# Performance work log

Hardware: AMD Instinct MI355X
Metric: run time of the kernel (lower is better)

Reference implementation:

```python
import jax, jax.numpy as jnp
import numpy as np

MARGIN = 0.3
K_AN = 3
K_AP = 6
KMAX = max(K_AN, K_AP)
NORMALIZE = True


def setup_inputs() -> dict:
    key = jax.random.key(0)
    k1, k2 = jax.random.split(key)
    inputs = jax.random.normal(k1, (128, 32, 128), dtype=jnp.float32)
    targets = jax.random.randint(k2, (128,), 0, 16, dtype=jnp.int64)
    return {"inputs": inputs, "targets": targets}


def _pair_stats(xi, xj):
    # xi, xj: (s, d) L2-normalized features of two tracklets
    s = xi.shape[0]
    xc = jnp.concatenate([xi, xj], axis=0)                     # (m, d), m = 2s
    sq = jnp.sum(xc * xc, axis=1)                              # (m,)
    dist = sq[:, None] + sq[None, :] - 2.0 * (xc @ xc.T)       # (m, m)
    dist = jnp.sqrt(jnp.clip(dist, 1e-12))
    # softmax over full m x m, THEN slice the cross block [0:s, s:m]
    row = jax.nn.softmax(dist, axis=1)[:s, s:]                 # (s, s)
    col = jax.nn.softmax(dist, axis=0)[:s, s:]                 # (s, s)
    a = jnp.min(row, axis=1)                                   # (s,) per-row mins
    c = jnp.min(col, axis=0)                                   # (s,) per-col mins
    ta = jax.lax.top_k(a, KMAX)[0]                             # sorted descending
    tc = jax.lax.top_k(c, KMAX)[0]
    v_same = jnp.maximum(ta[K_AP - 1], tc[K_AP - 1])           # k_ap-th largest
    v_diff = jnp.minimum(ta[K_AN - 1], tc[K_AN - 1])           # k_an-th largest
    return v_same, v_diff


def _loss(inputs, targets):
    b = inputs.shape[0]
    x = inputs
    if NORMALIZE:
        nrm = jnp.linalg.norm(x, axis=-1, keepdims=True)
        x = x / jnp.clip(nrm, 1e-12)
    # all-pairs stats: (b, b) each
    v_same, v_diff = jax.vmap(lambda xi: jax.vmap(lambda xj: _pair_stats(xi, xj))(x))(x)
    mask = targets[:, None] == targets[None, :]
    D = jnp.where(mask, v_same, v_diff)
    eye = jnp.eye(b, dtype=bool)
    D = jnp.where(eye, 0.0, D)                                 # torch loop leaves diag = 0
    dist_ap = jnp.max(jnp.where(mask, D, -jnp.inf), axis=1)    # hardest positive (incl. diag 0)
    dist_an = jnp.min(jnp.where(mask, jnp.inf, D), axis=1)     # hardest negative
    # MarginRankingLoss(margin)(an, ap, y=1) = mean(relu(ap - an + margin))
    return jnp.mean(jax.nn.relu(dist_ap - dist_an + MARGIN))


def reference(inputs, targets):
    return _loss(inputs, targets)
```

## Files before the change

### kernel.cpp

```cpp
#include <hip/hip_runtime.h>
#include <math.h>

#define B 128
#define S 32
#define Dm 128
#define NV (B * S)
#define MARGINF 0.3f
#define NTILE 2080
#define GRIDP 1040

#define K2F 2.0813689810056077f
#define C2F 4.1627379620112154f
#define EPS2 2.081368981e-12f

typedef __attribute__((ext_vector_type(8))) short short8;
typedef __attribute__((ext_vector_type(16))) float f32x16;

#define GLOBAL_AS __attribute__((address_space(1)))
#define LDS_AS __attribute__((address_space(3)))

#define FSQRT(x) __builtin_amdgcn_sqrtf(x)

__device__ inline float exp2raw(float x) {
    float r;
    asm("v_exp_f32 %0, %1" : "=v"(r) : "v"(x));
    return r;
}

__device__ inline unsigned short f2bf(float f) {
    unsigned u = __float_as_uint(f);
    unsigned r = u + 0x7FFF + ((u >> 16) & 1);
    return (unsigned short)(r >> 16);
}
__device__ inline float bf2f(unsigned short h) {
    return __uint_as_float(((unsigned)h) << 16);
}

__global__ __launch_bounds__(256) void prep_kernel(const float* __restrict__ X,
                                                   unsigned short* __restrict__ Zn,
                                                   float* __restrict__ sqv,
                                                   float* __restrict__ diagsum) {
    int i = blockIdx.x;
    __shared__ unsigned short zlds[4096];
    __shared__ float sq_sh[32];
    int t = threadIdx.x;

    int v = t >> 3;
    int s = t & 7;
    const float4* row = (const float4*)(X + (((size_t)i * S + v) << 7));

    float4 f[4];
    float ss = 0.f;
#pragma unroll
    for (int k = 0; k < 4; ++k) {
        f[k] = row[k * 8 + s];
        ss += f[k].x * f[k].x + f[k].y * f[k].y + f[k].z * f[k].z + f[k].w * f[k].w;
    }
    ss += __shfl_xor(ss, 1); ss += __shfl_xor(ss, 2); ss += __shfl_xor(ss, 4);
    float inv = 1.0f / fmaxf(FSQRT(ss), 1e-12f);

    float s2 = 0.f;
    unsigned short* zrow = Zn + (((size_t)i * S + v) << 7);
#pragma unroll
    for (int k = 0; k < 4; ++k) {
        int fidx = k * 8 + s;
        ushort4 h;
        h.x = f2bf(f[k].x * inv); h.y = f2bf(f[k].y * inv);
        h.z = f2bf(f[k].z * inv); h.w = f2bf(f[k].w * inv);
        float gx = bf2f(h.x), gy = bf2f(h.y), gz = bf2f(h.z), gw = bf2f(h.w);
        s2 += gx * gx + gy * gy + gz * gz + gw * gw;
        *(ushort4*)(zrow + fidx * 4) = h;
        int addr = (v << 8) + ((((fidx >> 1) ^ (v & 7))) << 4) + ((fidx & 1) << 3);
        *(ushort4*)((char*)zlds + addr) = h;
    }
    s2 += __shfl_xor(s2, 1); s2 += __shfl_xor(s2, 2); s2 += __shfl_xor(s2, 4);
    float s2s = s2 * K2F;
    if (s == 0) { sqv[(i << 5) + v] = s2s; sq_sh[v] = s2s; }
    __syncthreads();

    if (t < 64) {
        int lq = t & 31, kh = t >> 5, sx = lq & 7;
        f32x16 acc;
#pragma unroll
        for (int r = 0; r < 16; ++r) acc[r] = 0.f;
#pragma unroll
        for (int ks = 0; ks < 8; ++ks) {
            int off = (lq << 8) + (((2 * ks + kh) ^ sx) << 4);
            short8 av = *(const short8*)((char*)zlds + off);
            acc = __builtin_amdgcn_mfma_f32_32x32x16_bf16(av, av, acc, 0, 0, 0);
        }
        float sql = sq_sh[lq];
        float ssum = 0.f;
#pragma unroll
        for (int r = 0; r < 16; ++r) {
            int m = (r & 3) + 8 * (r >> 2) + 4 * kh;
            float d2 = fmaxf(sq_sh[m] + sql - C2F * acc[r], EPS2);
            ssum += exp2raw(FSQRT(d2));
        }
        ssum += __shfl_xor(ssum, 32);
        if (t < 32) diagsum[(i << 5) + lq] = ssum;
    }
}

__global__ __launch_bounds__(256) void pair_kernel(const unsigned short* __restrict__ Zn,
                                                   const float* __restrict__ sqv,
                                                   const float* __restrict__ diagsum,
                                                   const int* __restrict__ tgt,
                                                   float* __restrict__ Dmat) {
    extern __shared__ unsigned short lds[];

    int t = threadIdx.x;
    int w = t >> 6;
    int lane = t & 63;
    int slot = lane & 15;
    int rhi = lane >> 4;
    int lq = lane & 31;
    int kh = lane >> 5;
    int sx = lq & 7;

    for (int t0 = blockIdx.x; t0 < NTILE; t0 += GRIDP) {
        int jg = (int)((sqrtf(8.f * (float)t0 + 1.f) - 1.f) * 0.25f);
        while (jg > 0 && t0 < 2 * jg * jg + jg) --jg;
        while (t0 >= 2 * (jg + 1) * (jg + 1) + (jg + 1)) ++jg;
        int i = t0 - (2 * jg * jg + jg);
        int jbase = jg * 4;

        if (t0 != (int)blockIdx.x) __syncthreads();

#pragma unroll
        for (int k = 0; k < 10; ++k) {
            int seg = w * 10 + k;
            int panel = seg >> 3;
            int row = ((seg & 7) << 2) | rhi;
            int vec = (panel == 0) ? i : (jbase + panel - 1);
            const unsigned short* gsrc =
                Zn + ((size_t)vec << 12) + (row << 7) + ((slot ^ (row & 7)) << 3);
            unsigned short* ldst = lds + seg * 512;
            __builtin_amdgcn_global_load_lds((const GLOBAL_AS void*)(const void*)gsrc,
                                             (LDS_AS void*)(void*)ldst, 16, 0, 0);
        }
        __syncthreads();

        int j = jbase + w;
        if (j <= i) continue;

        const unsigned short* Pi = lds;
        const unsigned short* Pj = lds + (w + 1) * 4096;

        f32x16 acc, acc2;
#pragma unroll
        for (int r = 0; r < 16; ++r) { acc[r] = 0.f; acc2[r] = 0.f; }

#pragma unroll
        for (int ks = 0; ks < 8; ++ks) {
            int off = (lq << 7) + (((2 * ks + kh) ^ sx) << 3);
            short8 av = *(const short8*)(Pi + off);
            short8 bv = *(const short8*)(Pj + off);
            acc  = __builtin_amdgcn_mfma_f32_32x32x16_bf16(av, bv, acc, 0, 0, 0);
            acc2 = __builtin_amdgcn_mfma_f32_32x32x16_bf16(bv, av, acc2, 0, 0, 0);
        }

        float sqi_l = sqv[(i << 5) + lq];
        float sqj_l = sqv[(j << 5) + lq];
        float di = diagsum[(i << 5) + lq];
        float dj = diagsum[(j << 5) + lq];

        float sqa[16], sqb[16];
#pragma unroll
        for (int r = 0; r < 16; ++r) {
            int m = (r & 3) + 8 * (r >> 2) + 4 * kh;
            sqa[r] = __shfl(sqi_l, m);
            sqb[r] = __shfl(sqj_l, m);
        }

        float csum = 0.f, cmin = INFINITY, rsum = 0.f, rmin = INFINITY;
#pragma unroll
        for (int r = 0; r < 16; ++r) {
            float d2a = fmaxf(sqa[r] + sqj_l - C2F * acc[r], EPS2);
            float ea = exp2raw(FSQRT(d2a));
            csum += ea; cmin = fminf(cmin, ea);
            float d2b = fmaxf(sqi_l + sqb[r] - C2F * acc2[r], EPS2);
            float eb = exp2raw(FSQRT(d2b));
            rsum += eb; rmin = fminf(rmin, eb);
        }
        csum += __shfl_xor(csum, 32);
        cmin = fminf(cmin, __shfl_xor(cmin, 32));
        rsum += __shfl_xor(rsum, 32);
        rmin = fminf(rmin, __shfl_xor(rmin, 32));

        float aval = rmin / (di + rsum);
        float cval = cmin / (dj + csum);

        float v = (lane < 32) ? aval : cval;
#pragma unroll
        for (int k = 2; k <= 32; k <<= 1) {
#pragma unroll
            for (int mm = k >> 1; mm >= 1; mm >>= 1) {
                float o = __shfl_xor(v, mm);
                bool asc = ((lq & k) == 0);
                bool upper = (lq & mm) != 0;
                float mn = fminf(v, o), mx = fmaxf(v, o);
                v = (asc == upper) ? mx : mn;
            }
        }
        float ta3 = __shfl(v, 29), ta6 = __shfl(v, 26);
        float tc3 = __shfl(v, 61), tc6 = __shfl(v, 58);

        if (lane == 0) {
            float v_same = fmaxf(ta6, tc6);
            float v_diff = fminf(ta3, tc3);
            float val = (tgt[i] == tgt[j]) ? v_same : v_diff;
            Dmat[i * B + j] = val;
            Dmat[j * B + i] = val;
        }
    }
}

__global__ __launch_bounds__(1024) void final_kernel(const float* __restrict__ Dmat,
                                                     const int* __restrict__ tgt,
                                                     float* __restrict__ out) {
    int t = threadIdx.x;
    int i = t >> 3;
    int c = t & 7;
    int ti = tgt[i];
    float ap = -INFINITY, an = INFINITY;
#pragma unroll
    for (int k = 0; k < 16; ++k) {
        int jj = c * 16 + k;
        float v = (jj == i) ? 0.f : Dmat[jj * B + i];
        if (tgt[jj] == ti) ap = fmaxf(ap, v);
        else an = fminf(an, v);
    }
    ap = fmaxf(ap, __shfl_xor(ap, 1)); an = fminf(an, __shfl_xor(an, 1));
    ap = fmaxf(ap, __shfl_xor(ap, 2)); an = fminf(an, __shfl_xor(an, 2));
    ap = fmaxf(ap, __shfl_xor(ap, 4)); an = fminf(an, __shfl_xor(an, 4));

    __shared__ float red[128];
    if (c == 0) {
        float term = ap - an + MARGINF;
        red[i] = term > 0.f ? term : 0.f;
    }
    __syncthreads();
    if (t < 64) {
        float r0 = red[t] + red[t + 64];
        r0 += __shfl_down(r0, 32); r0 += __shfl_down(r0, 16);
        r0 += __shfl_down(r0, 8);  r0 += __shfl_down(r0, 4);
        r0 += __shfl_down(r0, 2);  r0 += __shfl_down(r0, 1);
        if (t == 0) out[0] = r0 / (float)B;
    }
}

extern "C" void kernel_launch(void* const* d_in, const int* in_sizes, int n_in,
                              void* d_out, int out_size, void* d_ws, size_t ws_size,
                              hipStream_t stream) {
    const float* X = (const float*)d_in[0];
    const int* tgt = (const int*)d_in[1];
    float* out = (float*)d_out;

    unsigned short* Zn = (unsigned short*)d_ws;
    float* sqv = (float*)(Zn + (size_t)NV * Dm);
    float* diagsum = sqv + NV;
    float* Dmat = diagsum + NV;

    prep_kernel<<<B, 256, 0, stream>>>(X, Zn, sqv, diagsum);
    pair_kernel<<<GRIDP, 256, 40960, stream>>>(Zn, sqv, diagsum, tgt, Dmat);
    final_kernel<<<1, 1024, 0, stream>>>(Dmat, tgt, out);
}
```

Measured before the change: 35.85 us.

## Fuse final reduction into pair kernel via atomics and last-block completion

Removes the separate final kernel and the D matrix. Each tile now atomically folds its value into per-row hardest-positive and hardest-negative arrays, using unsigned compare on non-negative float bits. The last block to finish, found through an atomic counter, computes the mean loss. This saves one kernel launch and a global round trip, at the cost of atomic contention and a fence-free last-block pattern. It also pre-adds the squared norms during the shuffle stage.

Measured after the change: 66.94 us. +86.7%, slower.

```diff
diff --git a/kernel.cpp b/kernel.cpp
--- a/kernel.cpp
+++ b/kernel.cpp
@@ -39,11 +39,19 @@
 __global__ __launch_bounds__(256) void prep_kernel(const float* __restrict__ X,
                                                    unsigned short* __restrict__ Zn,
                                                    float* __restrict__ sqv,
-                                                   float* __restrict__ diagsum) {
+                                                   float* __restrict__ diagsum,
+                                                   unsigned* __restrict__ apU,
+                                                   unsigned* __restrict__ anU,
+                                                   unsigned* __restrict__ cnt) {
     int i = blockIdx.x;
     __shared__ unsigned short zlds[4096];
     __shared__ float sq_sh[32];
     int t = threadIdx.x;
+    if (t == 0) {
+        apU[i] = 0u;
+        anU[i] = 0x7f800000u;
+        if (i == 0) cnt[0] = 0u;
+    }
 
     int v = t >> 3;
     int s = t & 7;
@@ -106,7 +114,10 @@
                                                    const float* __restrict__ sqv,
                                                    const float* __restrict__ diagsum,
                                                    const int* __restrict__ tgt,
-                                                   float* __restrict__ Dmat) {
+                                                   unsigned* __restrict__ apU,
+                                                   unsigned* __restrict__ anU,
+                                                   unsigned* __restrict__ cnt,
+                                                   float* __restrict__ out) {
     extern __shared__ unsigned short lds[];
 
     int t = threadIdx.x;
@@ -165,21 +176,21 @@
         float di = diagsum[(i << 5) + lq];
         float dj = diagsum[(j << 5) + lq];
 
-        float sqa[16], sqb[16];
+        float sab[16], sba[16];
 #pragma unroll
         for (int r = 0; r < 16; ++r) {
             int m = (r & 3) + 8 * (r >> 2) + 4 * kh;
-            sqa[r] = __shfl(sqi_l, m);
-            sqb[r] = __shfl(sqj_l, m);
+            sab[r] = __shfl(sqi_l, m) + sqj_l;
+            sba[r] = __shfl(sqj_l, m) + sqi_l;
         }
 
         float csum = 0.f, cmin = INFINITY, rsum = 0.f, rmin = INFINITY;
 #pragma unroll
         for (int r = 0; r < 16; ++r) {
-            float d2a = fmaxf(sqa[r] + sqj_l - C2F * acc[r], EPS2);
+            float d2a = fmaxf(sab[r] - C2F * acc[r], EPS2);
             float ea = exp2raw(FSQRT(d2a));
             csum += ea; cmin = fminf(cmin, ea);
-            float d2b = fmaxf(sqi_l + sqb[r] - C2F * acc2[r], EPS2);
+            float d2b = fmaxf(sba[r] - C2F * acc2[r], EPS2);
             float eb = exp2raw(FSQRT(d2b));
             rsum += eb; rmin = fminf(rmin, eb);
         }
@@ -209,44 +220,43 @@
         if (lane == 0) {
             float v_same = fmaxf(ta6, tc6);
             float v_diff = fminf(ta3, tc3);
-            float val = (tgt[i] == tgt[j]) ? v_same : v_diff;
-            Dmat[i * B + j] = val;
-            Dmat[j * B + i] = val;
-        }
-    }
-}
-
-__global__ __launch_bounds__(1024) void final_kernel(const float* __restrict__ Dmat,
-                                                     const int* __restrict__ tgt,
-                                                     float* __restrict__ out) {
-    int t = threadIdx.x;
-    int i = t >> 3;
-    int c = t & 7;
-    int ti = tgt[i];
-    float ap = -INFINITY, an = INFINITY;
-#pragma unroll
-    for (int k = 0; k < 16; ++k) {
-        int jj = c * 16 + k;
-        float v = (jj == i) ? 0.f : Dmat[jj * B + i];
-        if (tgt[jj] == ti) ap = fmaxf(ap, v);
-        else an = fminf(an, v);
-    }
-    ap = fmaxf(ap, __shfl_xor(ap, 1)); an = fminf(an, __shfl_xor(an, 1));
-    ap = fmaxf(ap, __shfl_xor(ap, 2)); an = fminf(an, __shfl_xor(an, 2));
-    ap = fmaxf(ap, __shfl_xor(ap, 4)); an = fminf(an, __shfl_xor(an, 4));
-
-    __shared__ float red[128];
-    if (c == 0) {
-        float term = ap - an + MARGINF;
-        red[i] = term > 0.f ? term : 0.f;
-    }
+            if (tgt[i] == tgt[j]) {
+                unsigned uv = __float_as_uint(v_same);
+                atomicMax(apU + i, uv);
+                atomicMax(apU + j, uv);
+            } else {
+                unsigned uv = __float_as_uint(v_diff);
+                atomicMin(anU + i, uv);
+                atomicMin(anU + j, uv);
+            }
+        }
+    }
+
     __syncthreads();
-    if (t < 64) {
-        float r0 = red[t] + red[t + 64];
-        r0 += __shfl_down(r0, 32); r0 += __shfl_down(r0, 16);
-        r0 += __shfl_down(r0, 8);  r0 += __shfl_down(r0, 4);
-        r0 += __shfl_down(r0, 2);  r0 += __shfl_down(r0, 1);
-        if (t == 0) out[0] = r0 / (float)B;
+    volatile unsigned* flag = (volatile unsigned*)lds;
+    if (t == 0) {
+        unsigned old = atomicAdd(cnt, 1u);
+        flag[0] = (old == GRIDP - 1) ? 1u : 0u;
+    }
+    __syncthreads();
+    if (flag[0]) {
+        float* red = (float*)lds + 64;
+        if (t < B) {
+            unsigned a = __hip_atomic_load(apU + t, __ATOMIC_RELAXED,
+                                           __HIP_MEMORY_SCOPE_AGENT);
+            unsigned n = __hip_atomic_load(anU + t, __ATOMIC_RELAXED,
+                                           __HIP_MEMORY_SCOPE_AGENT);
+            float term = __uint_as_float(a) - __uint_as_float(n) + MARGINF;
+            red[t] = term > 0.f ? term : 0.f;
+        }
+        __syncthreads();
+        if (t < 64) {
+            float r0 = red[t] + red[t + 64];
+            r0 += __shfl_down(r0, 32); r0 += __shfl_down(r0, 16);
+            r0 += __shfl_down(r0, 8);  r0 += __shfl_down(r0, 4);
+            r0 += __shfl_down(r0, 2);  r0 += __shfl_down(r0, 1);
+            if (t == 0) out[0] = r0 / (float)B;
+        }
     }
 }
 
@@ -260,9 +270,11 @@
     unsigned short* Zn = (unsigned short*)d_ws;
     float* sqv = (float*)(Zn + (size_t)NV * Dm);
     float* diagsum = sqv + NV;
-    float* Dmat = diagsum + NV;
-
-    prep_kernel<<<B, 256, 0, stream>>>(X, Zn, sqv, diagsum);
-    pair_kernel<<<GRIDP, 256, 40960, stream>>>(Zn, sqv, diagsum, tgt, Dmat);
-    final_kernel<<<1, 1024, 0, stream>>>(Dmat, tgt, out);
-}
+    unsigned* apU = (unsigned*)(diagsum + NV);
+    unsigned* anU = apU + B;
+    unsigned* cnt = anU + B;
+
+    prep_kernel<<<B, 256, 0, stream>>>(X, Zn, sqv, diagsum, apU, anU, cnt);
+    pair_kernel<<<GRIDP, 256, 40960, stream>>>(Zn, sqv, diagsum, tgt,
+                                               apU, anU, cnt, out);
+}
```

## Tile pair kernel as 2x4 blocks with 512 threads, one tile per block

Applied to the files above, without the earlier changes.

The pair kernel now covers a 2 i-vectors by 4 j-vectors tile per block, using 8 waves that share 6 LDS panels instead of 5 panels per 4 pairs. The persistent loop over two tiles per block is removed, so 1056 blocks each handle one tile. This reduces global-to-LDS loads per pair and the total tile count, and it also folds the squared-norm sums into the shuffle loop. In exchange, blocks are larger and more waves may exit early on diagonal tiles where j<=i.

Result: faster. 31.43 us, median of 2 (-12.3%).

```diff
diff --git a/kernel.cpp b/kernel.cpp
--- a/kernel.cpp
+++ b/kernel.cpp
@@ -6,8 +6,7 @@
 #define Dm 128
 #define NV (B * S)
 #define MARGINF 0.3f
-#define NTILE 2080
-#define GRIDP 1040
+#define NTILE 1056
 
 #define K2F 2.0813689810056077f
 #define C2F 4.1627379620112154f
@@ -102,11 +101,19 @@
     }
 }
 
-__global__ __launch_bounds__(256) void pair_kernel(const unsigned short* __restrict__ Zn,
+__global__ __launch_bounds__(512) void pair_kernel(const unsigned short* __restrict__ Zn,
                                                    const float* __restrict__ sqv,
                                                    const float* __restrict__ diagsum,
                                                    const int* __restrict__ tgt,
                                                    float* __restrict__ Dmat) {
+    int t0 = blockIdx.x;
+    int jg = (int)((sqrtf(4.f * (float)t0 + 1.f) - 1.f) * 0.5f);
+    while (jg > 0 && t0 < jg * jg + jg) --jg;
+    while (t0 >= (jg + 1) * (jg + 1) + (jg + 1)) ++jg;
+    int ip = t0 - (jg * jg + jg);
+    int i0 = ip * 2;
+    int jbase = jg * 4;
+
     extern __shared__ unsigned short lds[];
 
     int t = threadIdx.x;
@@ -114,105 +121,96 @@
     int lane = t & 63;
     int slot = lane & 15;
     int rhi = lane >> 4;
+
+#pragma unroll
+    for (int k = 0; k < 6; ++k) {
+        int seg = w * 6 + k;
+        int panel = seg >> 3;
+        int row = ((seg & 7) << 2) | rhi;
+        int vec = (panel < 2) ? (i0 + panel) : (jbase + panel - 2);
+        const unsigned short* gsrc =
+            Zn + ((size_t)vec << 12) + (row << 7) + ((slot ^ (row & 7)) << 3);
+        unsigned short* ldst = lds + seg * 512;
+        __builtin_amdgcn_global_load_lds((const GLOBAL_AS void*)(const void*)gsrc,
+                                         (LDS_AS void*)(void*)ldst, 16, 0, 0);
+    }
+    __syncthreads();
+
+    int i = i0 + (w >> 2);
+    int j = jbase + (w & 3);
+    if (j <= i) return;
+
+    const unsigned short* Pi = lds + (w >> 2) * 4096;
+    const unsigned short* Pj = lds + (2 + (w & 3)) * 4096;
     int lq = lane & 31;
     int kh = lane >> 5;
     int sx = lq & 7;
 
-    for (int t0 = blockIdx.x; t0 < NTILE; t0 += GRIDP) {
-        int jg = (int)((sqrtf(8.f * (float)t0 + 1.f) - 1.f) * 0.25f);
-        while (jg > 0 && t0 < 2 * jg * jg + jg) --jg;
-        while (t0 >= 2 * (jg + 1) * (jg + 1) + (jg + 1)) ++jg;
-        int i = t0 - (2 * jg * jg + jg);
-        int jbase = jg * 4;
-
-        if (t0 != (int)blockIdx.x) __syncthreads();
-
-#pragma unroll
-        for (int k = 0; k < 10; ++k) {
-            int seg = w * 10 + k;
-            int panel = seg >> 3;
-            int row = ((seg & 7) << 2) | rhi;
-            int vec = (panel == 0) ? i : (jbase + panel - 1);
-            const unsigned short* gsrc =
-                Zn + ((size_t)vec << 12) + (row << 7) + ((slot ^ (row & 7)) << 3);
-            unsigned short* ldst = lds + seg * 512;
-            __builtin_amdgcn_global_load_lds((const GLOBAL_AS void*)(const void*)gsrc,
-                                             (LDS_AS void*)(void*)ldst, 16, 0, 0);
+    f32x16 acc, acc2;
+#pragma unroll
+    for (int r = 0; r < 16; ++r) { acc[r] = 0.f; acc2[r] = 0.f; }
+
+#pragma unroll
+    for (int ks = 0; ks < 8; ++ks) {
+        int off = (lq << 7) + (((2 * ks + kh) ^ sx) << 3);
+        short8 av = *(const short8*)(Pi + off);
+        short8 bv = *(const short8*)(Pj + off);
+        acc  = __builtin_amdgcn_mfma_f32_32x32x16_bf16(av, bv, acc, 0, 0, 0);
+        acc2 = __builtin_amdgcn_mfma_f32_32x32x16_bf16(bv, av, acc2, 0, 0, 0);
+    }
+
+    float sqi_l = sqv[(i << 5) + lq];
+    float sqj_l = sqv[(j << 5) + lq];
+    float di = diagsum[(i << 5) + lq];
+    float dj = diagsum[(j << 5) + lq];
+
+    float sab[16], sba[16];
+#pragma unroll
+    for (int r = 0; r < 16; ++r) {
+        int m = (r & 3) + 8 * (r >> 2) + 4 * kh;
+        sab[r] = __shfl(sqi_l, m) + sqj_l;
+        sba[r] = __shfl(sqj_l, m) + sqi_l;
+    }
+
+    float csum = 0.f, cmin = INFINITY, rsum = 0.f, rmin = INFINITY;
+#pragma unroll
+    for (int r = 0; r < 16; ++r) {
+        float d2a = fmaxf(sab[r] - C2F * acc[r], EPS2);
+        float ea = exp2raw(FSQRT(d2a));
+        csum += ea; cmin = fminf(cmin, ea);
+        float d2b = fmaxf(sba[r] - C2F * acc2[r], EPS2);
+        float eb = exp2raw(FSQRT(d2b));
+        rsum += eb; rmin = fminf(rmin, eb);
+    }
+    csum += __shfl_xor(csum, 32);
+    cmin = fminf(cmin, __shfl_xor(cmin, 32));
+    rsum += __shfl_xor(rsum, 32);
+    rmin = fminf(rmin, __shfl_xor(rmin, 32));
+
+    float aval = rmin / (di + rsum);
+    float cval = cmin / (dj + csum);
+
+    float v = (lane < 32) ? aval : cval;
+#pragma unroll
+    for (int k = 2; k <= 32; k <<= 1) {
+#pragma unroll
+        for (int mm = k >> 1; mm >= 1; mm >>= 1) {
+            float o = __shfl_xor(v, mm);
+            bool asc = ((lq & k) == 0);
+            bool upper = (lq & mm) != 0;
+            float mn = fminf(v, o), mx = fmaxf(v, o);
+            v = (asc == upper) ? mx : mn;
         }
-        __syncthreads();
-
-        int j = jbase + w;
-        if (j <= i) continue;
-
-        const unsigned short* Pi = lds;
-        const unsigned short* Pj = lds + (w + 1) * 4096;
-
-        f32x16 acc, acc2;
-#pragma unroll
-        for (int r = 0; r < 16; ++r) { acc[r] = 0.f; acc2[r] = 0.f; }
-
-#pragma unroll
-        for (int ks = 0; ks < 8; ++ks) {
-            int off = (lq << 7) + (((2 * ks + kh) ^ sx) << 3);
-            short8 av = *(const short8*)(Pi + off);
-            short8 bv = *(const short8*)(Pj + off);
-            acc  = __builtin_amdgcn_mfma_f32_32x32x16_bf16(av, bv, acc, 0, 0, 0);
-            acc2 = __builtin_amdgcn_mfma_f32_32x32x16_bf16(bv, av, acc2, 0, 0, 0);
-        }
-
-        float sqi_l = sqv[(i << 5) + lq];
-        float sqj_l = sqv[(j << 5) + lq];
-        float di = diagsum[(i << 5) + lq];
-        float dj = diagsum[(j << 5) + lq];
-
-        float sqa[16], sqb[16];
-#pragma unroll
-        for (int r = 0; r < 16; ++r) {
-            int m = (r & 3) + 8 * (r >> 2) + 4 * kh;
-            sqa[r] = __shfl(sqi_l, m);
-            sqb[r] = __shfl(sqj_l, m);
-        }
-
-        float csum = 0.f, cmin = INFINITY, rsum = 0.f, rmin = INFINITY;
-#pragma unroll
-        for (int r = 0; r < 16; ++r) {
-            float d2a = fmaxf(sqa[r] + sqj_l - C2F * acc[r], EPS2);
-            float ea = exp2raw(FSQRT(d2a));
-            csum += ea; cmin = fminf(cmin, ea);
-            float d2b = fmaxf(sqi_l + sqb[r] - C2F * acc2[r], EPS2);
-            float eb = exp2raw(FSQRT(d2b));
-            rsum += eb; rmin = fminf(rmin, eb);
-        }
-        csum += __shfl_xor(csum, 32);
-        cmin = fminf(cmin, __shfl_xor(cmin, 32));
-        rsum += __shfl_xor(rsum, 32);
-        rmin = fminf(rmin, __shfl_xor(rmin, 32));
-
-        float aval = rmin / (di + rsum);
-        float cval = cmin / (dj + csum);
-
-        float v = (lane < 32) ? aval : cval;
-#pragma unroll
-        for (int k = 2; k <= 32; k <<= 1) {
-#pragma unroll
-            for (int mm = k >> 1; mm >= 1; mm >>= 1) {
-                float o = __shfl_xor(v, mm);
-                bool asc = ((lq & k) == 0);
-                bool upper = (lq & mm) != 0;
-                float mn = fminf(v, o), mx = fmaxf(v, o);
-                v = (asc == upper) ? mx : mn;
-            }
-        }
-        float ta3 = __shfl(v, 29), ta6 = __shfl(v, 26);
-        float tc3 = __shfl(v, 61), tc6 = __shfl(v, 58);
-
-        if (lane == 0) {
-            float v_same = fmaxf(ta6, tc6);
-            float v_diff = fminf(ta3, tc3);
-            float val = (tgt[i] == tgt[j]) ? v_same : v_diff;
-            Dmat[i * B + j] = val;
-            Dmat[j * B + i] = val;
-        }
+    }
+    float ta3 = __shfl(v, 29), ta6 = __shfl(v, 26);
+    float tc3 = __shfl(v, 61), tc6 = __shfl(v, 58);
+
+    if (lane == 0) {
+        float v_same = fmaxf(ta6, tc6);
+        float v_diff = fminf(ta3, tc3);
+        float val = (tgt[i] == tgt[j]) ? v_same : v_diff;
+        Dmat[i * B + j] = val;
+        Dmat[j * B + i] = val;
     }
 }
 
@@ -263,6 +261,7 @@
     float* Dmat = diagsum + NV;
 
     prep_kernel<<<B, 256, 0, stream>>>(X, Zn, sqv, diagsum);
-    pair_kernel<<<GRIDP, 256, 40960, stream>>>(Zn, sqv, diagsum, tgt, Dmat);
+    pair_kernel<<<NTILE, 512, 6 * 4096 * sizeof(unsigned short), stream>>>(
+        Zn, sqv, diagsum, tgt, Dmat);
     final_kernel<<<1, 1024, 0, stream>>>(Dmat, tgt, out);
 }
```
